# Performance work log

Measured on AMD Instinct MI355X. Metric: run time of the kernel, lower is better.

Reference implementation:

```python
import jax, jax.numpy as jnp
import numpy as np

BSZ, SEQ, HID = 8, 4096, 1024
N_EXPERTS = 8
CAPACITY = 512  # expert_capacity_per_batch; effective cap = min(SEQ, CAPACITY)
SCALE = 1.0     # routed_scaling_factor


def setup_inputs() -> dict:
    key = jax.random.key(0)
    k1, k2 = jax.random.split(key)
    hidden_states = jax.random.normal(k1, (BSZ, SEQ, HID), dtype=jnp.float32)
    # kaiming_uniform_(a=sqrt(5)) on [d,e] -> bound = 1/sqrt(fan_in=d)
    bound = 1.0 / np.sqrt(HID)
    weight = jax.random.uniform(k2, (HID, N_EXPERTS), dtype=jnp.float32,
                                minval=-bound, maxval=bound)
    return {"hidden_states": hidden_states, "weight": weight}


def reference(hidden_states, weight):
    bsz, seq_len, h = hidden_states.shape
    # gating logits in fp32: [b, s, e]
    logits = jnp.einsum('bsd,de->bse', hidden_states.astype(jnp.float32),
                        weight.astype(jnp.float32))
    affinity = jax.nn.softmax(logits, axis=-1)          # [b, s, e]
    affinity = jnp.transpose(affinity, (0, 2, 1))       # [b, e, s]
    cap = min(seq_len, CAPACITY)                        # static
    # Each expert picks its top-`cap` tokens (sorted descending, like torch.topk)
    topk_scores, topk_indices = jax.lax.top_k(affinity, cap)  # [b, e, cap]
    topk_scores = topk_scores * SCALE
    # dense dispatch mask [b, e, cap, s]: one-hot over token positions
    dispatch_mask = jax.nn.one_hot(topk_indices, seq_len, dtype=jnp.float32)
    return topk_indices, topk_scores, dispatch_mask
```

## Files before the change

kernel.cpp:

```cpp
#include <hip/hip_runtime.h>

constexpr int BSZ = 8, SEQ = 4096, HID = 1024, NE = 8, CAP = 512;
constexpr int ROWS = BSZ * NE;
constexpr size_t IDX_ELEMS = (size_t)ROWS * CAP;
constexpr size_t SCR_OFF = IDX_ELEMS;
constexpr size_t MASK_OFF = IDX_ELEMS * 2;
constexpr size_t MASK_ELEMS = (size_t)ROWS * CAP * SEQ;
constexpr size_t AFF_ELEMS = (size_t)ROWS * SEQ;
constexpr size_t AFF_BYTES = AFF_ELEMS * sizeof(float);
constexpr size_t KEYS_BYTES = (size_t)ROWS * SEQ * 8;

typedef float f4v __attribute__((ext_vector_type(4)));

__global__ __launch_bounds__(128) void gating_kernel(const float* __restrict__ hidden,
                                                     const float* __restrict__ weight,
                                                     float* __restrict__ aff)
{
    __shared__ float hls[16][68];
    __shared__ float wls[8][68];
    __shared__ float lls[16][8];

    const int tid = threadIdx.x;
    const int T0 = blockIdx.x * 16;
    const int t = tid >> 3;
    const int e = tid & 7;

    float v0 = 0.f, v1 = 0.f, v2 = 0.f, v3 = 0.f;
    for (int c = 0; c < 16; ++c) {
        __syncthreads();
#pragma unroll
        for (int k = 0; k < 2; ++k) {
            const int j = tid + k * 128;
            const int tt = j >> 4, q = j & 15;
            const float4 v = *(const float4*)(hidden + (size_t)(T0 + tt) * HID + c * 64 + 4 * q);
            *(float4*)&hls[tt][4 * q] = v;
        }
#pragma unroll
        for (int k = 0; k < 4; ++k) {
            const int j = tid + k * 128;
            const int dd = j >> 3, ee = j & 7;
            wls[ee][dd] = weight[(size_t)(c * 64 + dd) * NE + ee];
        }
        __syncthreads();
#pragma unroll
        for (int k = 0; k < 4; ++k) {
            const int base = 16 * k;
            const float4 hA = *(const float4*)&hls[t][base + 0];
            const float4 hB = *(const float4*)&hls[t][base + 4];
            const float4 hC = *(const float4*)&hls[t][base + 8];
            const float4 hD = *(const float4*)&hls[t][base + 12];
            const float4 wA = *(const float4*)&wls[e][base + 0];
            const float4 wB = *(const float4*)&wls[e][base + 4];
            const float4 wC = *(const float4*)&wls[e][base + 8];
            const float4 wD = *(const float4*)&wls[e][base + 12];
            v0 = __fadd_rn(__fmul_rn(hA.x, wA.x),
                 __fadd_rn(__fmul_rn(hB.x, wB.x),
                 __fadd_rn(__fmul_rn(hC.x, wC.x),
                 __fadd_rn(__fmul_rn(hD.x, wD.x), v0))));
            v1 = __fadd_rn(__fmul_rn(hA.y, wA.y),
                 __fadd_rn(__fmul_rn(hB.y, wB.y),
                 __fadd_rn(__fmul_rn(hC.y, wC.y),
                 __fadd_rn(__fmul_rn(hD.y, wD.y), v1))));
            v2 = __fadd_rn(__fmul_rn(hA.z, wA.z),
                 __fadd_rn(__fmul_rn(hB.z, wB.z),
                 __fadd_rn(__fmul_rn(hC.z, wC.z),
                 __fadd_rn(__fmul_rn(hD.z, wD.z), v2))));
            v3 = __fadd_rn(__fmul_rn(hA.w, wA.w),
                 __fadd_rn(__fmul_rn(hB.w, wB.w),
                 __fadd_rn(__fmul_rn(hC.w, wC.w),
                 __fadd_rn(__fmul_rn(hD.w, wD.w), v3))));
        }
    }
    const float logit = __fadd_rn(__fadd_rn(v0, v1), __fadd_rn(v2, v3));

    lls[t][e] = logit;
    __syncthreads();

    float l[8];
#pragma unroll
    for (int k = 0; k < 8; ++k) l[k] = lls[t][k];
    float m = l[0];
#pragma unroll
    for (int k = 1; k < 8; ++k) m = fmaxf(m, l[k]);
    float p[8];
#pragma unroll
    for (int k = 0; k < 8; ++k)
        p[k] = (float)exp((double)__fsub_rn(l[k], m));
    const float s = __fadd_rn(__fadd_rn(__fadd_rn(p[0], p[1]), __fadd_rn(p[2], p[3])),
                              __fadd_rn(__fadd_rn(p[4], p[5]), __fadd_rn(p[6], p[7])));
    const float a = __fdiv_rn(p[e], s);

    const int token = T0 + t;
    const int b = token >> 12;
    const int sidx = token & (SEQ - 1);
    aff[((size_t)b * NE + e) * SEQ + sidx] = a;
}

__global__ __launch_bounds__(256) void segsort_zero_kernel(const float* __restrict__ aff,
                                                           unsigned long long* __restrict__ keys,
                                                           float* __restrict__ out)
{
    __shared__ unsigned long long k[512];
    if (blockIdx.x < 512) {
        const int row = blockIdx.x >> 3, seg = blockIdx.x & 7;
        const int g0 = seg * 512;
        const float* a = aff + (size_t)row * SEQ + g0;
        for (int j = threadIdx.x; j < 512; j += 256) {
            const unsigned int fb = __float_as_uint(a[j]);
            k[j] = ((unsigned long long)fb << 32) | (unsigned int)(SEQ - 1 - (g0 + j));
        }
        for (int len = 2; len <= 512; len <<= 1) {
            for (int stride = len >> 1; stride > 0; stride >>= 1) {
                __syncthreads();
                const int t = threadIdx.x;
                const int i = (t << 1) - (t & (stride - 1));
                const int j = i + stride;
                const unsigned long long ki = k[i], kj = k[j];
                const bool desc = ((i & len) == 0);
                if (desc ? (ki < kj) : (ki > kj)) { k[i] = kj; k[j] = ki; }
            }
        }
        __syncthreads();
        unsigned long long* dst = keys + (size_t)row * SEQ + g0;
        for (int j = threadIdx.x; j < 512; j += 256) dst[j] = k[j];
    } else {
        const long long nz4 = (long long)(MASK_ELEMS >> 2);
        f4v* mz = (f4v*)(out + MASK_OFF);
        const f4v z4 = {0.f, 0.f, 0.f, 0.f};
        const long long stride = (long long)(2048 - 512) * 256;
        for (long long i = (long long)(blockIdx.x - 512) * 256 + threadIdx.x;
             i < nz4; i += stride)
            __builtin_nontemporal_store(z4, mz + i);
    }
}

__global__ __launch_bounds__(512) void merge_scatter_kernel(const unsigned long long* __restrict__ keys,
                                                            float* __restrict__ out)
{
    __shared__ unsigned long long A[SEQ];
    const int row = blockIdx.x;
    for (int i = threadIdx.x; i < SEQ; i += 512)
        A[i] = keys[(size_t)row * SEQ + i];

    for (int round = 0; round < 3; ++round) {
        const int sp = 1024 << round;
        const int npairs = 4 >> round;
        __syncthreads();
        for (int u = threadIdx.x; u < npairs * 512; u += 512) {
            const int p = u >> 9, i = u & 511;
            const int base = p * sp;
            const unsigned long long x = A[base + i];
            const unsigned long long y = A[base + sp / 2 + 511 - i];
            if (y > x) A[base + i] = y;
        }
        for (int s = 256; s > 0; s >>= 1) {
            __syncthreads();
            for (int u = threadIdx.x; u < npairs * 256; u += 512) {
                const int r = u >> 8, t2 = u & 255;
                const int base = r * sp;
                const int i = (t2 << 1) - (t2 & (s - 1));
                const unsigned long long x = A[base + i], y = A[base + i + s];
                if (y > x) { A[base + i] = y; A[base + i + s] = x; }
            }
        }
    }
    __syncthreads();
    if (threadIdx.x < CAP) {
        const int t = threadIdx.x;
        const unsigned long long k = A[t];
        const int idx = (SEQ - 1) - (int)(unsigned int)(k & 0xffffffffu);
        out[(size_t)row * CAP + t] = (float)idx;
        out[SCR_OFF + (size_t)row * CAP + t] =
            __uint_as_float((unsigned int)(k >> 32));
        out[MASK_OFF + ((size_t)row * CAP + t) * SEQ + idx] = 1.0f;
    }
}

__global__ __launch_bounds__(1024) void sortzero_kernel(const float* __restrict__ aff,
                                                        float* __restrict__ out)
{
    __shared__ unsigned long long keys[SEQ];
    const int row = blockIdx.x;
    const float* a = aff + (size_t)row * SEQ;
    float* mrow = out + MASK_OFF + (size_t)row * CAP * SEQ;

    for (int i = threadIdx.x; i < SEQ; i += 1024) {
        const unsigned int fb = __float_as_uint(a[i]);
        keys[i] = ((unsigned long long)fb << 32) | (unsigned int)(SEQ - 1 - i);
    }
    f4v* mz = (f4v*)mrow;
    const f4v z4 = {0.f, 0.f, 0.f, 0.f};
    int zi = 0;
    for (int len = 2; len <= SEQ; len <<= 1) {
        for (int stride = len >> 1; stride > 0; stride >>= 1) {
            __syncthreads();
#pragma unroll
            for (int k = 0; k < 7; ++k) {
                if (zi < 512) {
                    __builtin_nontemporal_store(z4, mz + (size_t)zi * 1024 + threadIdx.x);
                    ++zi;
                }
            }
            for (int t = threadIdx.x; t < SEQ / 2; t += 1024) {
                const int i = (t << 1) - (t & (stride - 1));
                const int j = i + stride;
                const unsigned long long ki = keys[i], kj = keys[j];
                const bool desc = ((i & len) == 0);
                if (desc ? (ki < kj) : (ki > kj)) { keys[i] = kj; keys[j] = ki; }
            }
        }
    }
    __syncthreads();
    if (threadIdx.x < CAP) {
        const int t = threadIdx.x;
        const unsigned long long k = keys[t];
        const int idx = (SEQ - 1) - (int)(unsigned int)(k & 0xffffffffu);
        out[(size_t)row * CAP + t] = (float)idx;
        out[SCR_OFF + (size_t)row * CAP + t] =
            __uint_as_float((unsigned int)(k >> 32));
        mrow[(size_t)t * SEQ + idx] = 1.0f;
    }
}

__global__ __launch_bounds__(1024) void topk_zero_kernel(const float* __restrict__ aff,
                                                         float* __restrict__ out,
                                                         long long zero_elems)
{
    __shared__ unsigned long long keys[SEQ];
    if (blockIdx.x < (unsigned)ROWS) {
        const int row = blockIdx.x;
        const float* a = aff + (size_t)row * SEQ;
        for (int i = threadIdx.x; i < SEQ; i += 1024) {
            const unsigned int fb = __float_as_uint(a[i]);
            keys[i] = ((unsigned long long)fb << 32) | (unsigned int)(SEQ - 1 - i);
        }
        for (int len = 2; len <= SEQ; len <<= 1) {
            for (int stride = len >> 1; stride > 0; stride >>= 1) {
                __syncthreads();
                for (int t = threadIdx.x; t < SEQ / 2; t += 1024) {
                    const int i = (t << 1) - (t & (stride - 1));
                    const int j = i + stride;
                    const unsigned long long ki = keys[i], kj = keys[j];
                    const bool desc = ((i & len) == 0);
                    if (desc ? (ki < kj) : (ki > kj)) { keys[i] = kj; keys[j] = ki; }
                }
            }
        }
        __syncthreads();
        if (threadIdx.x < CAP) {
            const int t = threadIdx.x;
            const unsigned long long k = keys[t];
            const int idx = (SEQ - 1) - (int)(unsigned int)(k & 0xffffffffu);
            out[(size_t)row * CAP + t] = (float)idx;
            out[SCR_OFF + (size_t)row * CAP + t] =
                __uint_as_float((unsigned int)(k >> 32));
        }
    } else {
        const long long nz4 = zero_elems >> 2;
        f4v* mz = (f4v*)(out + MASK_OFF);
        const f4v z4 = {0.f, 0.f, 0.f, 0.f};
        const long long stride = (long long)(gridDim.x - ROWS) * 1024;
        for (long long i = (long long)(blockIdx.x - ROWS) * 1024 + threadIdx.x;
             i < nz4; i += stride)
            __builtin_nontemporal_store(z4, mz + i);
    }
}

__global__ void tailzero_kernel(float* __restrict__ out)
{
    const long long n4 = (long long)(AFF_ELEMS >> 2);
    f4v* mz = (f4v*)(out + MASK_OFF + MASK_ELEMS - AFF_ELEMS);
    const f4v z4 = {0.f, 0.f, 0.f, 0.f};
    const long long i = (long long)blockIdx.x * blockDim.x + threadIdx.x;
    if (i < n4) __builtin_nontemporal_store(z4, mz + i);
}

__global__ void scatter_kernel(float* __restrict__ out)
{
    const int p = blockIdx.x * blockDim.x + threadIdx.x;
    if (p < (int)IDX_ELEMS) {
        const int idx = (int)out[p];
        out[MASK_OFF + (size_t)p * SEQ + idx] = 1.0f;
    }
}

extern "C" void kernel_launch(void* const* d_in, const int* in_sizes, int n_in,
                              void* d_out, int out_size, void* d_ws, size_t ws_size,
                              hipStream_t stream)
{
    const float* hidden = (const float*)d_in[0];
    const float* weight = (const float*)d_in[1];
    float* out = (float*)d_out;

    if (ws_size >= AFF_BYTES + KEYS_BYTES) {
        float* aff = (float*)d_ws;
        unsigned long long* keys = (unsigned long long*)((char*)d_ws + AFF_BYTES);
        gating_kernel<<<2048, 128, 0, stream>>>(hidden, weight, aff);
        segsort_zero_kernel<<<2048, 256, 0, stream>>>(aff, keys, out);
        merge_scatter_kernel<<<ROWS, 512, 0, stream>>>(keys, out);
    } else if (ws_size >= AFF_BYTES) {
        float* aff = (float*)d_ws;
        gating_kernel<<<2048, 128, 0, stream>>>(hidden, weight, aff);
        sortzero_kernel<<<ROWS, 1024, 0, stream>>>(aff, out);
    } else {
        float* aff = out + MASK_OFF + MASK_ELEMS - AFF_ELEMS;
        gating_kernel<<<2048, 128, 0, stream>>>(hidden, weight, aff);
        const long long zero_elems = (long long)(MASK_ELEMS - AFF_ELEMS);
        topk_zero_kernel<<<ROWS + 1984, 1024, 0, stream>>>(aff, out, zero_elems);
        tailzero_kernel<<<256, 256, 0, stream>>>(out);
        scatter_kernel<<<(int)((IDX_ELEMS + 255) / 256), 256, 0, stream>>>(out);
    }
}
```

Measured before the change: 649.0 us.

## Split mask zero-fill between gating and segment-sort kernels

Adds extra blocks to the gating kernel that zero the first five-eighths of the dense dispatch mask while the other blocks compute logits and softmax. The segment-sort kernel now zeroes only the remaining portion. The aim is to overlap the large store-bound zero fill with the memory-bound read of the hidden states, so bandwidth is used concurrently. The trade-off is contention between the two streams for HBM bandwidth, plus a fixed split ratio that may not match the real balance.

New measurement: 639.2 us. No clear change (-1.5%).

```diff
diff --git a/kernel.cpp b/kernel.cpp
--- a/kernel.cpp
+++ b/kernel.cpp
@@ -10,15 +10,29 @@
 constexpr size_t AFF_BYTES = AFF_ELEMS * sizeof(float);
 constexpr size_t KEYS_BYTES = (size_t)ROWS * SEQ * 8;
 
+constexpr long long NZ4_TOTAL = (long long)(MASK_ELEMS >> 2);
+constexpr long long Z_SPLIT   = NZ4_TOTAL * 5 / 8;
+
 typedef float f4v __attribute__((ext_vector_type(4)));
 
-__global__ __launch_bounds__(128) void gating_kernel(const float* __restrict__ hidden,
-                                                     const float* __restrict__ weight,
-                                                     float* __restrict__ aff)
+__global__ __launch_bounds__(128) void gatezero_kernel(const float* __restrict__ hidden,
+                                                       const float* __restrict__ weight,
+                                                       float* __restrict__ aff,
+                                                       float* __restrict__ out)
 {
     __shared__ float hls[16][68];
     __shared__ float wls[8][68];
     __shared__ float lls[16][8];
+
+    if (blockIdx.x >= 2048) {
+        f4v* mz = (f4v*)(out + MASK_OFF);
+        const f4v z4 = {0.f, 0.f, 0.f, 0.f};
+        const long long stride = (long long)(gridDim.x - 2048) * 128;
+        for (long long i = (long long)(blockIdx.x - 2048) * 128 + threadIdx.x;
+             i < Z_SPLIT; i += stride)
+            __builtin_nontemporal_store(z4, mz + i);
+        return;
+    }
 
     const int tid = threadIdx.x;
     const int T0 = blockIdx.x * 16;
@@ -124,12 +138,11 @@
         unsigned long long* dst = keys + (size_t)row * SEQ + g0;
         for (int j = threadIdx.x; j < 512; j += 256) dst[j] = k[j];
     } else {
-        const long long nz4 = (long long)(MASK_ELEMS >> 2);
         f4v* mz = (f4v*)(out + MASK_OFF);
         const f4v z4 = {0.f, 0.f, 0.f, 0.f};
-        const long long stride = (long long)(2048 - 512) * 256;
-        for (long long i = (long long)(blockIdx.x - 512) * 256 + threadIdx.x;
-             i < nz4; i += stride)
+        const long long stride = (long long)(gridDim.x - 512) * 256;
+        for (long long i = Z_SPLIT + (long long)(blockIdx.x - 512) * 256 + threadIdx.x;
+             i < NZ4_TOTAL; i += stride)
             __builtin_nontemporal_store(z4, mz + i);
     }
 }
@@ -174,6 +187,90 @@
             __uint_as_float((unsigned int)(k >> 32));
         out[MASK_OFF + ((size_t)row * CAP + t) * SEQ + idx] = 1.0f;
     }
+}
+
+__global__ __launch_bounds__(128) void gating_kernel(const float* __restrict__ hidden,
+                                                     const float* __restrict__ weight,
+                                                     float* __restrict__ aff)
+{
+    __shared__ float hls[16][68];
+    __shared__ float wls[8][68];
+    __shared__ float lls[16][8];
+
+    const int tid = threadIdx.x;
+    const int T0 = blockIdx.x * 16;
+    const int t = tid >> 3;
+    const int e = tid & 7;
+
+    float v0 = 0.f, v1 = 0.f, v2 = 0.f, v3 = 0.f;
+    for (int c = 0; c < 16; ++c) {
+        __syncthreads();
+#pragma unroll
+        for (int k = 0; k < 2; ++k) {
+            const int j = tid + k * 128;
+            const int tt = j >> 4, q = j & 15;
+            const float4 v = *(const float4*)(hidden + (size_t)(T0 + tt) * HID + c * 64 + 4 * q);
+            *(float4*)&hls[tt][4 * q] = v;
+        }
+#pragma unroll
+        for (int k = 0; k < 4; ++k) {
+            const int j = tid + k * 128;
+            const int dd = j >> 3, ee = j & 7;
+            wls[ee][dd] = weight[(size_t)(c * 64 + dd) * NE + ee];
+        }
+        __syncthreads();
+#pragma unroll
+        for (int k = 0; k < 4; ++k) {
+            const int base = 16 * k;
+            const float4 hA = *(const float4*)&hls[t][base + 0];
+            const float4 hB = *(const float4*)&hls[t][base + 4];
+            const float4 hC = *(const float4*)&hls[t][base + 8];
+            const float4 hD = *(const float4*)&hls[t][base + 12];
+            const float4 wA = *(const float4*)&wls[e][base + 0];
+            const float4 wB = *(const float4*)&wls[e][base + 4];
+            const float4 wC = *(const float4*)&wls[e][base + 8];
+            const float4 wD = *(const float4*)&wls[e][base + 12];
+            v0 = __fadd_rn(__fmul_rn(hA.x, wA.x),
+                 __fadd_rn(__fmul_rn(hB.x, wB.x),
+                 __fadd_rn(__fmul_rn(hC.x, wC.x),
+                 __fadd_rn(__fmul_rn(hD.x, wD.x), v0))));
+            v1 = __fadd_rn(__fmul_rn(hA.y, wA.y),
+                 __fadd_rn(__fmul_rn(hB.y, wB.y),
+                 __fadd_rn(__fmul_rn(hC.y, wC.y),
+                 __fadd_rn(__fmul_rn(hD.y, wD.y), v1))));
+            v2 = __fadd_rn(__fmul_rn(hA.z, wA.z),
+                 __fadd_rn(__fmul_rn(hB.z, wB.z),
+                 __fadd_rn(__fmul_rn(hC.z, wC.z),
+                 __fadd_rn(__fmul_rn(hD.z, wD.z), v2))));
+            v3 = __fadd_rn(__fmul_rn(hA.w, wA.w),
+                 __fadd_rn(__fmul_rn(hB.w, wB.w),
+                 __fadd_rn(__fmul_rn(hC.w, wC.w),
+                 __fadd_rn(__fmul_rn(hD.w, wD.w), v3))));
+        }
+    }
+    const float logit = __fadd_rn(__fadd_rn(v0, v1), __fadd_rn(v2, v3));
+
+    lls[t][e] = logit;
+    __syncthreads();
+
+    float l[8];
+#pragma unroll
+    for (int k = 0; k < 8; ++k) l[k] = lls[t][k];
+    float m = l[0];
+#pragma unroll
+    for (int k = 1; k < 8; ++k) m = fmaxf(m, l[k]);
+    float p[8];
+#pragma unroll
+    for (int k = 0; k < 8; ++k)
+        p[k] = (float)exp((double)__fsub_rn(l[k], m));
+    const float s = __fadd_rn(__fadd_rn(__fadd_rn(p[0], p[1]), __fadd_rn(p[2], p[3])),
+                              __fadd_rn(__fadd_rn(p[4], p[5]), __fadd_rn(p[6], p[7])));
+    const float a = __fdiv_rn(p[e], s);
+
+    const int token = T0 + t;
+    const int b = token >> 12;
+    const int sidx = token & (SEQ - 1);
+    aff[((size_t)b * NE + e) * SEQ + sidx] = a;
 }
 
 __global__ __launch_bounds__(1024) void sortzero_kernel(const float* __restrict__ aff,
@@ -295,8 +392,8 @@
     if (ws_size >= AFF_BYTES + KEYS_BYTES) {
         float* aff = (float*)d_ws;
         unsigned long long* keys = (unsigned long long*)((char*)d_ws + AFF_BYTES);
-        gating_kernel<<<2048, 128, 0, stream>>>(hidden, weight, aff);
-        segsort_zero_kernel<<<2048, 256, 0, stream>>>(aff, keys, out);
+        gatezero_kernel<<<2048 + 1920, 128, 0, stream>>>(hidden, weight, aff, out);
+        segsort_zero_kernel<<<512 + 1536, 256, 0, stream>>>(aff, keys, out);
         merge_scatter_kernel<<<ROWS, 512, 0, stream>>>(keys, out);
     } else if (ws_size >= AFF_BYTES) {
         float* aff = (float*)d_ws;
```
